# Kernel tuning notes

Measured on AMD Instinct MI355X. Metric: run time of the kernel, lower is better.

## Reference

```python
import jax, jax.numpy as jnp
import numpy as np

N = 100000        # num nodes
E = 1600000       # num edges
IN_DIM = 256
HID = 64          # per-head out_dim
OUT_DIM = 256
H = 4             # num heads
EDGE_DIM = 16
NEG_SLOPE = 0.2

def _xavier(key, shape):
    fan_in, fan_out = shape[-2], shape[-1]
    bound = float(np.sqrt(6.0 / (fan_in + fan_out)))
    return jax.random.uniform(key, shape, jnp.float32, -bound, bound)

def setup_inputs() -> dict:
    key = jax.random.key(0)
    ks = jax.random.split(key, 8)
    x = jax.random.normal(ks[0], (N, IN_DIM), jnp.float32)
    edge_index = jax.random.randint(ks[1], (2, E), 0, N, jnp.int64)
    edge_attr = jax.random.normal(ks[2], (E, EDGE_DIM), jnp.float32)
    W = _xavier(ks[3], (H, IN_DIM, HID))
    W_edge = _xavier(ks[4], (H, EDGE_DIM, HID))
    att = _xavier(ks[5], (H, 3 * HID, 1))[..., 0]          # [H, 3*HID]
    proj_w = _xavier(ks[6], (H * HID, OUT_DIM))
    proj_b = jnp.zeros((OUT_DIM,), jnp.float32)
    return {"x": x, "edge_index": edge_index, "edge_attr": edge_attr,
            "W": W, "W_edge": W_edge, "att": att,
            "proj_w": proj_w, "proj_b": proj_b}

def reference(x, edge_index, edge_attr, W, W_edge, att, proj_w, proj_b):
    src = edge_index[0]  # x_j (source) indices
    dst = edge_index[1]  # x_i (target) indices; softmax/aggregation segments

    # Per-head node transform: [H, N, HID]
    xw = jnp.einsum('ni,hio->hno', x, W)
    x_i = xw[:, dst]                                  # [H, E, HID]
    x_j = xw[:, src]                                  # [H, E, HID]
    edge_proj = jnp.einsum('ed,hdo->heo', edge_attr, W_edge)  # [H, E, HID]

    a1, a2, a3 = att[:, :HID], att[:, HID:2*HID], att[:, 2*HID:]  # [H, HID] each
    e = (jnp.einsum('heo,ho->he', x_i, a1)
         + jnp.einsum('heo,ho->he', x_j, a2)
         + jnp.einsum('heo,ho->he', edge_proj, a3))   # [H, E]
    e = jnp.where(e >= 0, e, NEG_SLOPE * e)           # LeakyReLU

    def seg_softmax(eh):  # eh: [E]
        m = jax.ops.segment_max(eh, dst, num_segments=N)
        m = jnp.where(jnp.isfinite(m), m, 0.0)
        ex = jnp.exp(eh - m[dst])
        s = jax.ops.segment_sum(ex, dst, num_segments=N)
        return ex / (s[dst] + 1e-16)

    alpha = jax.vmap(seg_softmax)(e)                  # [H, E]  (dropout: eval mode)

    msg = x_j * alpha[..., None]                      # [H, E, HID]
    out_h = jax.vmap(lambda m: jax.ops.segment_sum(m, dst, num_segments=N))(msg)  # [H, N, HID]
    out = jnp.transpose(out_h, (1, 0, 2)).reshape(N, H * HID)  # concat heads
    out = out @ proj_w + proj_b
    return jax.nn.elu(out)
```

## Files before the change

### kernel.cpp

```cpp
#include <hip/hip_runtime.h>
#include <hip/hip_bf16.h>
#include <stdint.h>

#define N_NODES 100000
#define E_EDGES 1600000
#define NEG_SLOPE 0.2f
#define NBUCK 1563
#define BK_SH 6
#define CAP 1536

typedef short short8 __attribute__((ext_vector_type(8)));
typedef float f32x4 __attribute__((ext_vector_type(4)));

__device__ __forceinline__ unsigned short f2bf(float f) {
  union { float f; unsigned int u; } c; c.f = f;
  unsigned int u = c.u;
  unsigned int r = u + 0x7FFFu + ((u >> 16) & 1u);
  return (unsigned short)(r >> 16);
}
__device__ __forceinline__ float asf(unsigned int u) {
  union { unsigned int u; float f; } c; c.u = u;
  return c.f;
}

__global__ void k_detect(const void* ei, int* flag) {
  int t = threadIdx.x;
  int v = ((const int*)ei)[2 * t + 1];
  unsigned long long b = __ballot(v != 0);
  if (t == 0) *flag = (b != 0ull) ? 1 : 0;
}

__global__ void k_prep(const float* __restrict__ W, const float* __restrict__ proj_w,
                       const float* __restrict__ W_edge, const float* __restrict__ att,
                       unsigned short* __restrict__ Bt, unsigned short* __restrict__ Pt,
                       float* __restrict__ w3) {
  int t = blockIdx.x * 256 + threadIdx.x;
  if (t < 65536) {
    int col = t >> 8, k = t & 255;
    int h = col >> 6, o = col & 63;
    Bt[t] = f2bf(W[h * 16384 + k * 64 + o]);
  } else if (t < 131072) {
    int t2 = t - 65536;
    int o = t2 >> 8, i = t2 & 255;
    Pt[t2] = f2bf(proj_w[i * 256 + o]);
  } else if (t < 131136) {
    int t3 = t - 131072;
    int h = t3 >> 4, d = t3 & 15;
    float s = 0.f;
    for (int o = 0; o < 64; ++o)
      s += W_edge[h * 1024 + d * 64 + o] * att[h * 192 + 128 + o];
    w3[t3] = s;
  }
}

__global__ __launch_bounds__(256, 4) void k_gemm_x(const float* __restrict__ x,
    const unsigned short* __restrict__ Bt, const float* __restrict__ att,
    unsigned int* __restrict__ xwq, float* __restrict__ scl4,
    float* __restrict__ s1, float* __restrict__ s2) {
  __shared__ __align__(16) char smem[32768];
  unsigned short* As = (unsigned short*)smem;
  float* Ls = (float*)smem;
  float* attS = (float*)(smem + 24576);
  const int bm = blockIdx.x * 64;
  const int t = threadIdx.x;

#pragma unroll
  for (int i = 0; i < 16; ++i) {
    int c = i * 256 + t;
    int row = c >> 6, f4 = c & 63;
    uint2 w = make_uint2(0u, 0u);
    if (bm + row < N_NODES) {
      float4 v = *(const float4*)(x + (size_t)(bm + row) * 256 + f4 * 4);
      w.x = (unsigned int)f2bf(v.x) | ((unsigned int)f2bf(v.y) << 16);
      w.y = (unsigned int)f2bf(v.z) | ((unsigned int)f2bf(v.w) << 16);
    }
    int phys = row * 512 + (((f4 >> 1) ^ (row & 7)) << 4) + ((f4 & 1) << 3);
    *(uint2*)((char*)As + phys) = w;
  }
  __syncthreads();

  const int wave = t >> 6;
  const int lane = t & 63;
  const int l16 = lane & 15, lg = lane >> 4;
  const int colbase = wave * 64;
  f32x4 acc[4][4];
#pragma unroll
  for (int i = 0; i < 4; i++)
#pragma unroll
    for (int j = 0; j < 4; j++) acc[i][j] = (f32x4){0.f, 0.f, 0.f, 0.f};

  short8 bcur[4], bnxt[4];
#pragma unroll
  for (int ni = 0; ni < 4; ni++)
    bcur[ni] = *(const short8*)(Bt + (colbase + ni * 16 + l16) * 256 + lg * 8);

#pragma unroll
  for (int ks = 0; ks < 8; ++ks) {
    short8 a[4];
#pragma unroll
    for (int mi = 0; mi < 4; mi++) {
      int row = mi * 16 + l16;
      int phys = row * 512 + (((ks * 4 + lg) ^ (row & 7)) << 4);
      a[mi] = *(const short8*)((const char*)As + phys);
    }
    if (ks < 7) {
      const int k0n = (ks + 1) * 32 + lg * 8;
#pragma unroll
      for (int ni = 0; ni < 4; ni++)
        bnxt[ni] = *(const short8*)(Bt + (colbase + ni * 16 + l16) * 256 + k0n);
    }
#pragma unroll
    for (int mi = 0; mi < 4; mi++)
#pragma unroll
      for (int ni = 0; ni < 4; ni++)
        acc[mi][ni] = __builtin_amdgcn_mfma_f32_16x16x32_bf16(a[mi], bcur[ni], acc[mi][ni], 0, 0, 0);
#pragma unroll
    for (int ni = 0; ni < 4; ni++) bcur[ni] = bnxt[ni];
  }

  __syncthreads();
  for (int i = t; i < 768; i += 256) attS[i] = att[i];

  const int row16 = t >> 4;
  const int g = t & 15;
  const int h = g >> 2;
  const int cwh = (g & 3) * 16;
#pragma unroll
  for (int mi = 0; mi < 4; mi++) {
    __syncthreads();
#pragma unroll
    for (int r = 0; r < 4; r++)
#pragma unroll
      for (int ni = 0; ni < 4; ni++)
        Ls[(lg * 4 + r) * 260 + colbase + ni * 16 + l16] = acc[mi][ni][r];
    __syncthreads();
    float v[16];
#pragma unroll
    for (int k = 0; k < 4; ++k) {
      float4 f = *(const float4*)&Ls[row16 * 260 + g * 16 + k * 4];
      v[4 * k] = f.x; v[4 * k + 1] = f.y; v[4 * k + 2] = f.z; v[4 * k + 3] = f.w;
    }
    float mx = 0.f, p1 = 0.f, p2 = 0.f;
#pragma unroll
    for (int j = 0; j < 16; ++j) {
      mx = fmaxf(mx, fabsf(v[j]));
      p1 += v[j] * attS[h * 192 + cwh + j];
      p2 += v[j] * attS[h * 192 + 64 + cwh + j];
    }
    mx = fmaxf(mx, __shfl_xor(mx, 1, 64));
    mx = fmaxf(mx, __shfl_xor(mx, 2, 64));
    p1 += __shfl_xor(p1, 1, 64); p1 += __shfl_xor(p1, 2, 64);
    p2 += __shfl_xor(p2, 1, 64); p2 += __shfl_xor(p2, 2, 64);
    int row = bm + mi * 16 + row16;
    if (row < N_NODES) {
      mx += 1e-30f;
      float inv = 127.f / mx;
      uint4 pk;
      unsigned int* pw = &pk.x;
#pragma unroll
      for (int k = 0; k < 4; ++k) {
        int q0 = __float2int_rn(v[4 * k] * inv);
        int q1 = __float2int_rn(v[4 * k + 1] * inv);
        int q2 = __float2int_rn(v[4 * k + 2] * inv);
        int q3 = __float2int_rn(v[4 * k + 3] * inv);
        pw[k] = (q0 & 0xFF) | ((q1 & 0xFF) << 8) | ((q2 & 0xFF) << 16) |
                ((unsigned int)(q3 & 0xFF) << 24);
      }
      *(uint4*)(xwq + (size_t)row * 64 + g * 4) = pk;
      if ((g & 3) == 0) {
        scl4[row * 4 + h] = mx * (1.f / 127.f);
        s1[row * 4 + h] = p1;
        s2[row * 4 + h] = p2;
      }
    }
  }
}

__global__ __launch_bounds__(1024) void k_hist(const void* ei, const int* __restrict__ flag,
                                               int* __restrict__ bhist) {
  __shared__ int h[NBUCK];
  for (int i = threadIdx.x; i < NBUCK; i += 1024) h[i] = 0;
  __syncthreads();
  int f = *flag;
  int base = blockIdx.x * 4096;
#pragma unroll
  for (int k = 0; k < 4; ++k) {
    int e = base + k * 1024 + threadIdx.x;
    if (e < E_EDGES) {
      int dst = f ? ((const int*)ei)[E_EDGES + e] : (int)(((const long long*)ei)[E_EDGES + e]);
      atomicAdd(&h[dst >> BK_SH], 1);
    }
  }
  __syncthreads();
  for (int i = threadIdx.x; i < NBUCK; i += 1024) {
    int c = h[i];
    if (c) atomicAdd(&bhist[i], c);
  }
}

__global__ __launch_bounds__(1024) void k_scanb(const int* __restrict__ bhist,
                                                int* __restrict__ boff, int* __restrict__ bcur) {
  __shared__ int s[2048];
  int t = threadIdx.x;
  int ia = t, ib = t + 1024;
  int va = (ia < NBUCK) ? bhist[ia] : 0;
  int vb = (ib < NBUCK) ? bhist[ib] : 0;
  s[ia] = va; s[ib] = vb;
  __syncthreads();
  for (int off = 1; off < 2048; off <<= 1) {
    int xa = (ia >= off) ? s[ia - off] : 0;
    int xb = (ib >= off) ? s[ib - off] : 0;
    __syncthreads();
    s[ia] += xa; s[ib] += xb;
    __syncthreads();
  }
  if (ia < NBUCK) { boff[ia] = s[ia] - va; bcur[ia] = s[ia] - va; }
  if (ib < NBUCK) { boff[ib] = s[ib] - vb; bcur[ib] = s[ib] - vb; }
  if (t == 0) boff[NBUCK] = E_EDGES;
}

__global__ __launch_bounds__(1024) void k_edge(const void* ei, const int* __restrict__ flag,
                       const float* __restrict__ edge_attr,
                       const float* __restrict__ s1, const float* __restrict__ s2,
                       const float* __restrict__ w3g, int* __restrict__ bcur,
                       uint4* __restrict__ evs) {
  __shared__ float w3[64];
  __shared__ int cnt[NBUCK];
  __shared__ int rb[NBUCK];
  __shared__ int cur[NBUCK];
  const int t = threadIdx.x;
  for (int i = t; i < NBUCK; i += 1024) { cnt[i] = 0; cur[i] = 0; }
  if (t < 64) w3[t] = w3g[t];
  __syncthreads();

  const int f = *flag;
  const int base = blockIdx.x * 4096;
  int dstv[4], srcv[4];
  unsigned int pav[4], pbv[4];
#pragma unroll
  for (int k = 0; k < 4; ++k) {
    int e = base + k * 1024 + t;
    dstv[k] = -1;
    if (e < E_EDGES) {
      int src, dst;
      if (f) {
        src = ((const int*)ei)[e];
        dst = ((const int*)ei)[E_EDGES + e];
      } else {
        src = (int)(((const long long*)ei)[e]);
        dst = (int)(((const long long*)ei)[E_EDGES + e]);
      }
      float4 sd = *(const float4*)(s1 + (size_t)dst * 4);
      float4 ss = *(const float4*)(s2 + (size_t)src * 4);
      float ea[16];
#pragma unroll
      for (int i = 0; i < 4; i++) {
        float4 v = *(const float4*)(edge_attr + (size_t)e * 16 + i * 4);
        ea[4 * i] = v.x; ea[4 * i + 1] = v.y; ea[4 * i + 2] = v.z; ea[4 * i + 3] = v.w;
      }
      float ex[4];
#pragma unroll
      for (int h = 0; h < 4; h++) {
        float d = 0.f;
#pragma unroll
        for (int i = 0; i < 16; i++) d += ea[i] * w3[h * 16 + i];
        float v = (&sd.x)[h] + (&ss.x)[h] + d;
        v = (v >= 0.f) ? v : NEG_SLOPE * v;
        ex[h] = __expf(v);
      }
      dstv[k] = dst;
      srcv[k] = src;
      pav[k] = ((unsigned int)f2bf(ex[1]) << 16) | (unsigned int)f2bf(ex[0]);
      pbv[k] = ((unsigned int)f2bf(ex[3]) << 16) | (unsigned int)f2bf(ex[2]);
      atomicAdd(&cnt[dst >> BK_SH], 1);
    }
  }
  __syncthreads();
  for (int i = t; i < NBUCK; i += 1024) {
    int c = cnt[i];
    if (c) rb[i] = atomicAdd(&bcur[i], c);
  }
  __syncthreads();
#pragma unroll
  for (int k = 0; k < 4; ++k) {
    if (dstv[k] >= 0) {
      int bk = dstv[k] >> BK_SH;
      int pos = rb[bk] + atomicAdd(&cur[bk], 1);
      evs[pos] = make_uint4((unsigned int)srcv[k], pav[k], pbv[k],
                            (unsigned int)(dstv[k] & 63));
    }
  }
}

__global__ __launch_bounds__(256) void k_aggr(const int* __restrict__ boff,
    const uint4* __restrict__ evs, const unsigned int* __restrict__ xwq,
    const float* __restrict__ scl4, unsigned short* __restrict__ out_hb) {
  __shared__ int lsrc[CAP];
  __shared__ uint2 lw[CAP];
  __shared__ int cnt[64], bs[64], cur[64];
  const int b = blockIdx.x;
  const int t = threadIdx.x;
  const int e0 = boff[b];
  const int ne = boff[b + 1] - e0;
  if (t < 64) { cnt[t] = 0; cur[t] = 0; }
  __syncthreads();
  const bool ok = (ne <= CAP);
  if (ok) {
    uint4 rv[6];
#pragma unroll
    for (int k = 0; k < 6; ++k) {
      int i = k * 256 + t;
      if (i < ne) {
        rv[k] = evs[e0 + i];
        atomicAdd(&cnt[rv[k].w], 1);
      }
    }
    __syncthreads();
    if (t < 64) bs[t] = cnt[t];
    __syncthreads();
    for (int off = 1; off < 64; off <<= 1) {
      int x = 0;
      if (t < 64 && t >= off) x = bs[t - off];
      __syncthreads();
      if (t < 64) bs[t] += x;
      __syncthreads();
    }
#pragma unroll
    for (int k = 0; k < 6; ++k) {
      int i = k * 256 + t;
      if (i < ne) {
        int ld = rv[k].w;
        int slot = bs[ld] - cnt[ld] + atomicAdd(&cur[ld], 1);
        lsrc[slot] = (int)rv[k].x;
        lw[slot] = make_uint2(rv[k].y, rv[k].z);
      }
    }
    __syncthreads();
  }

  const int wv = t >> 6, lane = t & 63;
  const int hsel = lane >> 4;
  const bool hlo2 = (hsel < 2);
  const bool hodd = (hsel & 1);

#define EDGE_FMA(wv_, sc_, u_)                                            \
  {                                                                       \
    unsigned int wp = hlo2 ? (wv_).x : (wv_).y;                           \
    float wlo = asf(wp << 16), whi = asf(wp & 0xFFFF0000u);               \
    float w = hodd ? whi : wlo;                                           \
    den += w;                                                             \
    float ws = w * (sc_);                                                 \
    acc0 += ws * (float)(int)(signed char)((u_) & 0xFF);                  \
    acc1 += ws * (float)(int)(signed char)(((u_) >> 8) & 0xFF);           \
    acc2 += ws * (float)(int)(signed char)(((u_) >> 16) & 0xFF);          \
    acc3 += ws * (float)(int)(signed char)((u_) >> 24);                   \
  }

  for (int r = 0; r < 16; ++r) {
    const int ln = wv * 16 + r;
    const int n = b * 64 + ln;
    if (n >= N_NODES) break;
    float acc0 = 0.f, acc1 = 0.f, acc2 = 0.f, acc3 = 0.f, den = 0.f;
    if (ok) {
      const int je = bs[ln];
      int j = je - cnt[ln];
      for (; j + 4 <= je; j += 4) {
        int s0 = lsrc[j], s1_ = lsrc[j + 1], s2_ = lsrc[j + 2], s3_ = lsrc[j + 3];
        uint2 w0 = lw[j], w1 = lw[j + 1], w2 = lw[j + 2], w3_ = lw[j + 3];
        float c0 = scl4[(size_t)s0 * 4 + hsel];
        float c1 = scl4[(size_t)s1_ * 4 + hsel];
        float c2 = scl4[(size_t)s2_ * 4 + hsel];
        float c3 = scl4[(size_t)s3_ * 4 + hsel];
        unsigned int u0 = xwq[(size_t)s0 * 64 + lane];
        unsigned int u1 = xwq[(size_t)s1_ * 64 + lane];
        unsigned int u2 = xwq[(size_t)s2_ * 64 + lane];
        unsigned int u3 = xwq[(size_t)s3_ * 64 + lane];
        EDGE_FMA(w0, c0, u0);
        EDGE_FMA(w1, c1, u1);
        EDGE_FMA(w2, c2, u2);
        EDGE_FMA(w3_, c3, u3);
      }
      for (; j < je; ++j) {
        int s0 = lsrc[j];
        uint2 w0 = lw[j];
        float c0 = scl4[(size_t)s0 * 4 + hsel];
        unsigned int u0 = xwq[(size_t)s0 * 64 + lane];
        EDGE_FMA(w0, c0, u0);
      }
    } else {
      for (int i = 0; i < ne; ++i) {
        uint4 v0 = evs[e0 + i];
        if ((int)v0.w == ln) {
          uint2 w0 = make_uint2(v0.y, v0.z);
          float c0 = scl4[(size_t)v0.x * 4 + hsel];
          unsigned int u0 = xwq[(size_t)v0.x * 64 + lane];
          EDGE_FMA(w0, c0, u0);
        }
      }
    }
    float d = den + 1e-16f;
    uint2 o;
    o.x = ((unsigned int)f2bf(acc1 / d) << 16) | (unsigned int)f2bf(acc0 / d);
    o.y = ((unsigned int)f2bf(acc3 / d) << 16) | (unsigned int)f2bf(acc2 / d);
    *(uint2*)(out_hb + (size_t)n * 256 + lane * 4) = o;
  }
#undef EDGE_FMA
}

__global__ __launch_bounds__(256, 4) void k_gemm_out(const unsigned short* __restrict__ A,
    const unsigned short* __restrict__ Pt, const float* __restrict__ bias,
    float* __restrict__ out) {
  __shared__ __align__(16) char smem[32768];
  unsigned short* As = (unsigned short*)smem;
  float* Ls = (float*)smem;
  const int bm = blockIdx.x * 64;
  const int t = threadIdx.x;

#pragma unroll
  for (int i = 0; i < 8; ++i) {
    int c = i * 256 + t;
    int row = c >> 5, G = c & 31;
    short8 v = (short8){0, 0, 0, 0, 0, 0, 0, 0};
    if (bm + row < N_NODES) v = *(const short8*)(A + (size_t)(bm + row) * 256 + G * 8);
    int phys = row * 512 + ((G ^ (row & 7)) << 4);
    *(short8*)((char*)As + phys) = v;
  }
  __syncthreads();

  const int wave = t >> 6;
  const int lane = t & 63;
  const int l16 = lane & 15, lg = lane >> 4;
  const int colbase = wave * 64;
  f32x4 acc[4][4];
#pragma unroll
  for (int i = 0; i < 4; i++)
#pragma unroll
    for (int j = 0; j < 4; j++) acc[i][j] = (f32x4){0.f, 0.f, 0.f, 0.f};

  short8 bcur[4], bnxt[4];
#pragma unroll
  for (int ni = 0; ni < 4; ni++)
    bcur[ni] = *(const short8*)(Pt + (colbase + ni * 16 + l16) * 256 + lg * 8);

#pragma unroll
  for (int ks = 0; ks < 8; ++ks) {
    short8 a[4];
#pragma unroll
    for (int mi = 0; mi < 4; mi++) {
      int row = mi * 16 + l16;
      int phys = row * 512 + (((ks * 4 + lg) ^ (row & 7)) << 4);
      a[mi] = *(const short8*)((const char*)As + phys);
    }
    if (ks < 7) {
      const int k0n = (ks + 1) * 32 + lg * 8;
#pragma unroll
      for (int ni = 0; ni < 4; ni++)
        bnxt[ni] = *(const short8*)(Pt + (colbase + ni * 16 + l16) * 256 + k0n);
    }
#pragma unroll
    for (int mi = 0; mi < 4; mi++)
#pragma unroll
      for (int ni = 0; ni < 4; ni++)
        acc[mi][ni] = __builtin_amdgcn_mfma_f32_16x16x32_bf16(a[mi], bcur[ni], acc[mi][ni], 0, 0, 0);
#pragma unroll
    for (int ni = 0; ni < 4; ni++) bcur[ni] = bnxt[ni];
  }

  const int row16 = t >> 4;
  const int q = t & 15;
#pragma unroll
  for (int mi = 0; mi < 4; mi++) {
    __syncthreads();
#pragma unroll
    for (int r = 0; r < 4; r++) {
#pragma unroll
      for (int ni = 0; ni < 4; ni++)
        Ls[(lg * 4 + r) * 260 + colbase + ni * 16 + l16] = acc[mi][ni][r];
    }
    __syncthreads();
    int grow = bm + mi * 16 + row16;
    if (grow < N_NODES) {
#pragma unroll
      for (int k = 0; k < 4; ++k) {
        int qc = (q + k * 16) * 4;
        float4 v = *(const float4*)&Ls[row16 * 260 + qc];
        float4 bv = *(const float4*)(bias + qc);
        v.x += bv.x; v.y += bv.y; v.z += bv.z; v.w += bv.w;
        v.x = (v.x > 0.f) ? v.x : (__expf(v.x) - 1.f);
        v.y = (v.y > 0.f) ? v.y : (__expf(v.y) - 1.f);
        v.z = (v.z > 0.f) ? v.z : (__expf(v.z) - 1.f);
        v.w = (v.w > 0.f) ? v.w : (__expf(v.w) - 1.f);
        *(float4*)(out + (size_t)grow * 256 + qc) = v;
      }
    }
  }
}

extern "C" void kernel_launch(void* const* d_in, const int* in_sizes, int n_in,
                              void* d_out, int out_size, void* d_ws, size_t ws_size,
                              hipStream_t stream) {
  const float* x = (const float*)d_in[0];
  const void* ei = d_in[1];
  const float* edge_attr = (const float*)d_in[2];
  const float* W = (const float*)d_in[3];
  const float* W_edge = (const float*)d_in[4];
  const float* att = (const float*)d_in[5];
  const float* proj_w = (const float*)d_in[6];
  const float* proj_b = (const float*)d_in[7];
  float* out = (float*)d_out;

  char* ws = (char*)d_ws;
  size_t off = 0;
  auto alloc = [&](size_t bytes) -> void* {
    void* p = (void*)(ws + off);
    off += (bytes + 255) & ~(size_t)255;
    return p;
  };
  unsigned int* xwq     = (unsigned int*)alloc((size_t)N_NODES * 256);
  float* scl4    = (float*)alloc((size_t)N_NODES * 4 * 4);
  unsigned short* outhb = (unsigned short*)alloc((size_t)N_NODES * 256 * 2);
  float* s1      = (float*)alloc((size_t)N_NODES * 4 * 4);
  float* s2      = (float*)alloc((size_t)N_NODES * 4 * 4);
  uint4* evs     = (uint4*)alloc((size_t)E_EDGES * 16);
  int* bhist     = (int*)alloc((size_t)NBUCK * 4);
  int* boff      = (int*)alloc((size_t)(NBUCK + 1) * 4);
  int* bcur      = (int*)alloc((size_t)NBUCK * 4);
  unsigned short* Bt = (unsigned short*)alloc(65536 * 2);
  unsigned short* Pt = (unsigned short*)alloc(65536 * 2);
  float* w3      = (float*)alloc(64 * 4);
  int* flag      = (int*)alloc(256);

  const int NB_E = (E_EDGES + 4095) / 4096;

  hipMemsetAsync(bhist, 0, (size_t)NBUCK * 4, stream);
  k_detect<<<1, 64, 0, stream>>>(ei, flag);
  k_prep<<<(131136 + 255) / 256, 256, 0, stream>>>(W, proj_w, W_edge, att, Bt, Pt, w3);
  k_gemm_x<<<(N_NODES + 63) / 64, 256, 0, stream>>>(x, Bt, att, xwq, scl4, s1, s2);
  k_hist<<<NB_E, 1024, 0, stream>>>(ei, flag, bhist);
  k_scanb<<<1, 1024, 0, stream>>>(bhist, boff, bcur);
  k_edge<<<NB_E, 1024, 0, stream>>>(ei, flag, edge_attr, s1, s2, w3, bcur, evs);
  k_aggr<<<NBUCK, 256, 0, stream>>>(boff, evs, xwq, scl4, outhb);
  k_gemm_out<<<(N_NODES + 63) / 64, 256, 0, stream>>>(outhb, Pt, proj_b, out);
}
```

Baseline: 300.2 us.

## Fuse neighbor aggregation with output projection GEMM in one kernel

Merges the aggregation kernel and the output projection GEMM so each 64-node bucket writes its aggregated bf16 rows into a swizzled shared-memory tile and runs the MFMA projection straight away. This removes the global round trip of the N x 256 bf16 intermediate and one kernel launch. In exchange the block needs more shared memory (about 51 KB, occupancy hint 3) and carries more register pressure, which could lower the occupancy of the latency-bound gather phase.

```diff
diff --git a/kernel.cpp b/kernel.cpp
--- a/kernel.cpp
+++ b/kernel.cpp
@@ -292,12 +292,20 @@
   }
 }
 
-__global__ __launch_bounds__(256) void k_aggr(const int* __restrict__ boff,
+__global__ __launch_bounds__(256, 3) void k_aggr_proj(const int* __restrict__ boff,
     const uint4* __restrict__ evs, const unsigned int* __restrict__ xwq,
-    const float* __restrict__ scl4, unsigned short* __restrict__ out_hb) {
-  __shared__ int lsrc[CAP];
-  __shared__ uint2 lw[CAP];
-  __shared__ int cnt[64], bs[64], cur[64];
+    const float* __restrict__ scl4, const unsigned short* __restrict__ Pt,
+    const float* __restrict__ bias, float* __restrict__ out) {
+  __shared__ __align__(16) char smem[52224];
+  unsigned short* As = (unsigned short*)smem;
+  char* gbase = smem + 32768;
+  int* lsrc = (int*)gbase;
+  uint2* lw = (uint2*)(gbase + 6144);
+  int* cnt = (int*)(gbase + 18432);
+  int* bs  = (int*)(gbase + 18688);
+  int* cur = (int*)(gbase + 18944);
+  float* Ls = (float*)gbase;
+
   const int b = blockIdx.x;
   const int t = threadIdx.x;
   const int e0 = boff[b];
@@ -402,45 +410,25 @@
     uint2 o;
     o.x = ((unsigned int)f2bf(acc1 / d) << 16) | (unsigned int)f2bf(acc0 / d);
     o.y = ((unsigned int)f2bf(acc3 / d) << 16) | (unsigned int)f2bf(acc2 / d);
-    *(uint2*)(out_hb + (size_t)n * 256 + lane * 4) = o;
+    int phys = ln * 512 + ((((lane >> 1)) ^ (ln & 7)) << 4) + ((lane & 1) << 3);
+    *(uint2*)((char*)As + phys) = o;
   }
 #undef EDGE_FMA
-}
-
-__global__ __launch_bounds__(256, 4) void k_gemm_out(const unsigned short* __restrict__ A,
-    const unsigned short* __restrict__ Pt, const float* __restrict__ bias,
-    float* __restrict__ out) {
-  __shared__ __align__(16) char smem[32768];
-  unsigned short* As = (unsigned short*)smem;
-  float* Ls = (float*)smem;
-  const int bm = blockIdx.x * 64;
-  const int t = threadIdx.x;
-
-#pragma unroll
-  for (int i = 0; i < 8; ++i) {
-    int c = i * 256 + t;
-    int row = c >> 5, G = c & 31;
-    short8 v = (short8){0, 0, 0, 0, 0, 0, 0, 0};
-    if (bm + row < N_NODES) v = *(const short8*)(A + (size_t)(bm + row) * 256 + G * 8);
-    int phys = row * 512 + ((G ^ (row & 7)) << 4);
-    *(short8*)((char*)As + phys) = v;
-  }
-  __syncthreads();
-
-  const int wave = t >> 6;
-  const int lane = t & 63;
+
   const int l16 = lane & 15, lg = lane >> 4;
-  const int colbase = wave * 64;
+  const int colbase = wv * 64;
   f32x4 acc[4][4];
 #pragma unroll
   for (int i = 0; i < 4; i++)
 #pragma unroll
     for (int j = 0; j < 4; j++) acc[i][j] = (f32x4){0.f, 0.f, 0.f, 0.f};
 
-  short8 bcur[4], bnxt[4];
+  short8 bcur_[4], bnxt_[4];
 #pragma unroll
   for (int ni = 0; ni < 4; ni++)
-    bcur[ni] = *(const short8*)(Pt + (colbase + ni * 16 + l16) * 256 + lg * 8);
+    bcur_[ni] = *(const short8*)(Pt + (colbase + ni * 16 + l16) * 256 + lg * 8);
+
+  __syncthreads();
 
 #pragma unroll
   for (int ks = 0; ks < 8; ++ks) {
@@ -455,17 +443,18 @@
       const int k0n = (ks + 1) * 32 + lg * 8;
 #pragma unroll
       for (int ni = 0; ni < 4; ni++)
-        bnxt[ni] = *(const short8*)(Pt + (colbase + ni * 16 + l16) * 256 + k0n);
+        bnxt_[ni] = *(const short8*)(Pt + (colbase + ni * 16 + l16) * 256 + k0n);
     }
 #pragma unroll
     for (int mi = 0; mi < 4; mi++)
 #pragma unroll
       for (int ni = 0; ni < 4; ni++)
-        acc[mi][ni] = __builtin_amdgcn_mfma_f32_16x16x32_bf16(a[mi], bcur[ni], acc[mi][ni], 0, 0, 0);
-#pragma unroll
-    for (int ni = 0; ni < 4; ni++) bcur[ni] = bnxt[ni];
-  }
-
+        acc[mi][ni] = __builtin_amdgcn_mfma_f32_16x16x32_bf16(a[mi], bcur_[ni], acc[mi][ni], 0, 0, 0);
+#pragma unroll
+    for (int ni = 0; ni < 4; ni++) bcur_[ni] = bnxt_[ni];
+  }
+
+  const int bm = b * 64;
   const int row16 = t >> 4;
   const int q = t & 15;
 #pragma unroll
@@ -518,7 +507,6 @@
   };
   unsigned int* xwq     = (unsigned int*)alloc((size_t)N_NODES * 256);
   float* scl4    = (float*)alloc((size_t)N_NODES * 4 * 4);
-  unsigned short* outhb = (unsigned short*)alloc((size_t)N_NODES * 256 * 2);
   float* s1      = (float*)alloc((size_t)N_NODES * 4 * 4);
   float* s2      = (float*)alloc((size_t)N_NODES * 4 * 4);
   uint4* evs     = (uint4*)alloc((size_t)E_EDGES * 16);
@@ -539,6 +527,5 @@
   k_hist<<<NB_E, 1024, 0, stream>>>(ei, flag, bhist);
   k_scanb<<<1, 1024, 0, stream>>>(bhist, boff, bcur);
   k_edge<<<NB_E, 1024, 0, stream>>>(ei, flag, edge_attr, s1, s2, w3, bcur, evs);
-  k_aggr<<<NBUCK, 256, 0, stream>>>(boff, evs, xwq, scl4, outhb);
-  k_gemm_out<<<(N_NODES + 63) / 64, 256, 0, stream>>>(outhb, Pt, proj_b, out);
-}
+  k_aggr_proj<<<NBUCK, 256, 0, stream>>>(boff, evs, xwq, scl4, Pt, proj_b, out);
+}
```

Measured after the change: 316.5 us. +5.4%, slower.

## Replace histogram+scan bucketing with fixed-capacity buckets plus overflow list

Applied to the files above, without the earlier changes.

Removes the separate histogram and prefix-scan kernels. Edges are now scattered directly into fixed-capacity per-bucket slots (CAPS entries each), with any excess going to a global overflow array that every aggregation thread scans linearly. This saves one full pass over the edge indices and two launches. In exchange it uses more scratch memory, and the padded bucket layout adds some scatter sparsity. If overflow occurs, every node pays for the linear scan.

```diff
diff --git a/kernel.cpp b/kernel.cpp
--- a/kernel.cpp
+++ b/kernel.cpp
@@ -7,7 +7,9 @@
 #define NEG_SLOPE 0.2f
 #define NBUCK 1563
 #define BK_SH 6
+#define CAPS 2048
 #define CAP 1536
+#define OVF_MAX 8192
 
 typedef short short8 __attribute__((ext_vector_type(8)));
 typedef float f32x4 __attribute__((ext_vector_type(4)));
@@ -176,54 +178,12 @@
   }
 }
 
-__global__ __launch_bounds__(1024) void k_hist(const void* ei, const int* __restrict__ flag,
-                                               int* __restrict__ bhist) {
-  __shared__ int h[NBUCK];
-  for (int i = threadIdx.x; i < NBUCK; i += 1024) h[i] = 0;
-  __syncthreads();
-  int f = *flag;
-  int base = blockIdx.x * 4096;
-#pragma unroll
-  for (int k = 0; k < 4; ++k) {
-    int e = base + k * 1024 + threadIdx.x;
-    if (e < E_EDGES) {
-      int dst = f ? ((const int*)ei)[E_EDGES + e] : (int)(((const long long*)ei)[E_EDGES + e]);
-      atomicAdd(&h[dst >> BK_SH], 1);
-    }
-  }
-  __syncthreads();
-  for (int i = threadIdx.x; i < NBUCK; i += 1024) {
-    int c = h[i];
-    if (c) atomicAdd(&bhist[i], c);
-  }
-}
-
-__global__ __launch_bounds__(1024) void k_scanb(const int* __restrict__ bhist,
-                                                int* __restrict__ boff, int* __restrict__ bcur) {
-  __shared__ int s[2048];
-  int t = threadIdx.x;
-  int ia = t, ib = t + 1024;
-  int va = (ia < NBUCK) ? bhist[ia] : 0;
-  int vb = (ib < NBUCK) ? bhist[ib] : 0;
-  s[ia] = va; s[ib] = vb;
-  __syncthreads();
-  for (int off = 1; off < 2048; off <<= 1) {
-    int xa = (ia >= off) ? s[ia - off] : 0;
-    int xb = (ib >= off) ? s[ib - off] : 0;
-    __syncthreads();
-    s[ia] += xa; s[ib] += xb;
-    __syncthreads();
-  }
-  if (ia < NBUCK) { boff[ia] = s[ia] - va; bcur[ia] = s[ia] - va; }
-  if (ib < NBUCK) { boff[ib] = s[ib] - vb; bcur[ib] = s[ib] - vb; }
-  if (t == 0) boff[NBUCK] = E_EDGES;
-}
-
 __global__ __launch_bounds__(1024) void k_edge(const void* ei, const int* __restrict__ flag,
                        const float* __restrict__ edge_attr,
                        const float* __restrict__ s1, const float* __restrict__ s2,
                        const float* __restrict__ w3g, int* __restrict__ bcur,
-                       uint4* __restrict__ evs) {
+                       uint4* __restrict__ evs, uint4* __restrict__ ovf,
+                       int* __restrict__ ovfc) {
   __shared__ float w3[64];
   __shared__ int cnt[NBUCK];
   __shared__ int rb[NBUCK];
@@ -285,32 +245,47 @@
   for (int k = 0; k < 4; ++k) {
     if (dstv[k] >= 0) {
       int bk = dstv[k] >> BK_SH;
-      int pos = rb[bk] + atomicAdd(&cur[bk], 1);
-      evs[pos] = make_uint4((unsigned int)srcv[k], pav[k], pbv[k],
-                            (unsigned int)(dstv[k] & 63));
-    }
-  }
-}
-
-__global__ __launch_bounds__(256) void k_aggr(const int* __restrict__ boff,
-    const uint4* __restrict__ evs, const unsigned int* __restrict__ xwq,
+      int slot = rb[bk] + atomicAdd(&cur[bk], 1);
+      if (slot < CAPS) {
+        evs[(size_t)bk * CAPS + slot] = make_uint4((unsigned int)srcv[k], pav[k], pbv[k],
+                                                   (unsigned int)(dstv[k] & 63));
+      } else {
+        int oi = atomicAdd(ovfc, 1);
+        if (oi < OVF_MAX)
+          ovf[oi] = make_uint4((unsigned int)srcv[k], pav[k], pbv[k],
+                               (unsigned int)dstv[k]);
+      }
+    }
+  }
+}
+
+__global__ __launch_bounds__(256) void k_aggr(const int* __restrict__ bcur,
+    const uint4* __restrict__ evs, const uint4* __restrict__ ovf,
+    const int* __restrict__ ovfc, const unsigned int* __restrict__ xwq,
     const float* __restrict__ scl4, unsigned short* __restrict__ out_hb) {
   __shared__ int lsrc[CAP];
   __shared__ uint2 lw[CAP];
   __shared__ int cnt[64], bs[64], cur[64];
+  __shared__ int onS;
   const int b = blockIdx.x;
   const int t = threadIdx.x;
-  const int e0 = boff[b];
-  const int ne = boff[b + 1] - e0;
+  const size_t e0 = (size_t)b * CAPS;
+  const int ne = bcur[b];
+  const int stored = (ne < CAPS) ? ne : CAPS;
   if (t < 64) { cnt[t] = 0; cur[t] = 0; }
-  __syncthreads();
-  const bool ok = (ne <= CAP);
+  if (t == 0) {
+    int on = *ovfc;
+    onS = (on < 0) ? 0 : ((on > OVF_MAX) ? OVF_MAX : on);
+  }
+  __syncthreads();
+  const int on = onS;
+  const bool ok = (stored <= CAP);
   if (ok) {
     uint4 rv[6];
 #pragma unroll
     for (int k = 0; k < 6; ++k) {
       int i = k * 256 + t;
-      if (i < ne) {
+      if (i < stored) {
         rv[k] = evs[e0 + i];
         atomicAdd(&cnt[rv[k].w], 1);
       }
@@ -328,7 +303,7 @@
 #pragma unroll
     for (int k = 0; k < 6; ++k) {
       int i = k * 256 + t;
-      if (i < ne) {
+      if (i < stored) {
         int ld = rv[k].w;
         int slot = bs[ld] - cnt[ld] + atomicAdd(&cur[ld], 1);
         lsrc[slot] = (int)rv[k].x;
@@ -388,7 +363,7 @@
         EDGE_FMA(w0, c0, u0);
       }
     } else {
-      for (int i = 0; i < ne; ++i) {
+      for (int i = 0; i < stored; ++i) {
         uint4 v0 = evs[e0 + i];
         if ((int)v0.w == ln) {
           uint2 w0 = make_uint2(v0.y, v0.z);
@@ -396,6 +371,15 @@
           unsigned int u0 = xwq[(size_t)v0.x * 64 + lane];
           EDGE_FMA(w0, c0, u0);
         }
+      }
+    }
+    for (int i = 0; i < on; ++i) {
+      uint4 v0 = ovf[i];
+      if ((int)v0.w == n) {
+        uint2 w0 = make_uint2(v0.y, v0.z);
+        float c0 = scl4[(size_t)v0.x * 4 + hsel];
+        unsigned int u0 = xwq[(size_t)v0.x * 64 + lane];
+        EDGE_FMA(w0, c0, u0);
       }
     }
     float d = den + 1e-16f;
@@ -521,10 +505,10 @@
   unsigned short* outhb = (unsigned short*)alloc((size_t)N_NODES * 256 * 2);
   float* s1      = (float*)alloc((size_t)N_NODES * 4 * 4);
   float* s2      = (float*)alloc((size_t)N_NODES * 4 * 4);
-  uint4* evs     = (uint4*)alloc((size_t)E_EDGES * 16);
-  int* bhist     = (int*)alloc((size_t)NBUCK * 4);
-  int* boff      = (int*)alloc((size_t)(NBUCK + 1) * 4);
-  int* bcur      = (int*)alloc((size_t)NBUCK * 4);
+  uint4* evs     = (uint4*)alloc((size_t)NBUCK * CAPS * 16);
+  uint4* ovf     = (uint4*)alloc((size_t)OVF_MAX * 16);
+  int* bcur      = (int*)alloc((size_t)(NBUCK + 64) * 4);
+  int* ovfc      = bcur + NBUCK;
   unsigned short* Bt = (unsigned short*)alloc(65536 * 2);
   unsigned short* Pt = (unsigned short*)alloc(65536 * 2);
   float* w3      = (float*)alloc(64 * 4);
@@ -532,13 +516,11 @@
 
   const int NB_E = (E_EDGES + 4095) / 4096;
 
-  hipMemsetAsync(bhist, 0, (size_t)NBUCK * 4, stream);
+  hipMemsetAsync(bcur, 0, (size_t)(NBUCK + 64) * 4, stream);
   k_detect<<<1, 64, 0, stream>>>(ei, flag);
   k_prep<<<(131136 + 255) / 256, 256, 0, stream>>>(W, proj_w, W_edge, att, Bt, Pt, w3);
   k_gemm_x<<<(N_NODES + 63) / 64, 256, 0, stream>>>(x, Bt, att, xwq, scl4, s1, s2);
-  k_hist<<<NB_E, 1024, 0, stream>>>(ei, flag, bhist);
-  k_scanb<<<1, 1024, 0, stream>>>(bhist, boff, bcur);
-  k_edge<<<NB_E, 1024, 0, stream>>>(ei, flag, edge_attr, s1, s2, w3, bcur, evs);
-  k_aggr<<<NBUCK, 256, 0, stream>>>(boff, evs, xwq, scl4, outhb);
+  k_edge<<<NB_E, 1024, 0, stream>>>(ei, flag, edge_attr, s1, s2, w3, bcur, evs, ovf, ovfc);
+  k_aggr<<<NBUCK, 256, 0, stream>>>(bcur, evs, ovf, ovfc, xwq, scl4, outhb);
   k_gemm_out<<<(N_NODES + 63) / 64, 256, 0, stream>>>(outhb, Pt, proj_b, out);
 }
```

After: 293.1 us. 1.02x faster.
